# Kernel tuning notes

Hardware: AMD Instinct MI355X
Metric: run time of the kernel (lower is better)

Reference implementation:

```python
import jax, jax.numpy as jnp
import numpy as np

N_NODES, N_FEAT, N_HID, N_CLS = 50000, 128, 64, 16
N_EDGES, N_EDGES2 = 800000, 3000000


def _rand_edges(key, n_edges, n_nodes):
    # self-loop-free random edge list [2, E] (src, dst)
    k1, k2 = jax.random.split(key)
    src = jax.random.randint(k1, (n_edges,), 0, n_nodes)
    off = jax.random.randint(k2, (n_edges,), 1, n_nodes)
    dst = (src + off) % n_nodes
    return jnp.stack([src, dst]).astype(jnp.int64)


def setup_inputs() -> dict:
    key = jax.random.key(0)
    ks = jax.random.split(key, 8)
    x = jax.random.normal(ks[0], (N_NODES, N_FEAT), jnp.float32)
    edge_index = _rand_edges(ks[1], N_EDGES, N_NODES)    # original edges, no self loops
    edge_index2 = _rand_edges(ks[2], N_EDGES2, N_NODES)  # exclusive 2-hop edges
    w1 = jax.random.normal(ks[3], (N_FEAT, N_HID), jnp.float32) / np.sqrt(N_FEAT)
    b1 = jnp.zeros((N_HID,), jnp.float32)
    w2 = jax.random.normal(ks[4], (3 * N_HID, N_CLS), jnp.float32) / np.sqrt(3 * N_HID)
    b2 = jnp.zeros((N_CLS,), jnp.float32)
    lin_w = jax.random.normal(ks[5], (3 * N_CLS, N_CLS), jnp.float32) / np.sqrt(3 * N_CLS)
    lin_b = jnp.zeros((N_CLS,), jnp.float32)
    return {"x": x, "w1": w1, "b1": b1, "w2": w2, "b2": b2,
            "lin_w": lin_w, "lin_b": lin_b,
            "edge_index": edge_index, "edge_index2": edge_index2}


def _gcn_conv(h, W, b, ei, n):
    # PyG GCNConv(add_self_loops=False): transform, symmetric-normalize, scatter-add, bias.
    hw = h @ W                                   # [n, d_out]
    src, dst = ei[0], ei[1]
    ones = jnp.ones(ei.shape[1], h.dtype)
    deg = jax.ops.segment_sum(ones, dst, num_segments=n)       # in-degree
    dinv = jnp.where(deg > 0, jax.lax.rsqrt(jnp.maximum(deg, 1e-12)), 0.0)
    norm = dinv[src] * dinv[dst]                 # [E]
    msg = hw[src] * norm[:, None]                # gather + scale (traffic-bound)
    return jax.ops.segment_sum(msg, dst, num_segments=n) + b


def reference(x, w1, b1, w2, b2, lin_w, lin_b, edge_index, edge_index2):
    n = x.shape[0]
    # layer 1: three branches over (original edges, 2-hop edges, self-loop-only)
    h1 = _gcn_conv(x, w1, b1, edge_index, n)
    h1_2 = _gcn_conv(x, w1, b1, edge_index2, n)
    h1_3 = x @ w1 + b1                           # self-loop-only GCN: deg=1, norm=1
    R1 = jax.nn.relu(jnp.concatenate([h1, h1_2, h1_3], axis=1))  # dropout = identity (eval)
    # layer 2: same three branches with shared gcn2 weights
    h2 = _gcn_conv(R1, w2, b2, edge_index, n)
    h2_2 = _gcn_conv(R1, w2, b2, edge_index2, n)
    h2_3 = R1 @ w2 + b2
    R2 = jnp.concatenate([h2, h2_2, h2_3], axis=1)
    out = R2 @ lin_w + lin_b
    return jax.nn.log_softmax(out, axis=1)
```

## Files before the change

### kernel.cpp

```cpp
#include <hip/hip_runtime.h>
#include <math.h>


#define NPB    64
#define CHUNK  8192
#define HCHUNK 16384

typedef unsigned short us8 __attribute__((ext_vector_type(8)));

__device__ inline float b2f(unsigned short u) {
    return __uint_as_float(((unsigned int)u) << 16);
}
__device__ inline unsigned short f2b(float f) {
    unsigned int u = __float_as_uint(f);
    u = (u + 0x7FFFu + ((u >> 16) & 1u)) >> 16;
    return (unsigned short)u;
}

__global__ void __launch_bounds__(256)
k_gemm1(const float* __restrict__ x, const float* __restrict__ w1,
        unsigned short* __restrict__ hwb, int n) {
    __shared__ float ws[128 * 64];
    __shared__ float xs[64 * 128];
    int t = threadIdx.x;
    int row0 = blockIdx.x * 64;
    for (int i = t; i < 128 * 16; i += 256)
        ((float4*)ws)[i] = ((const float4*)w1)[i];
    for (int i = t; i < 64 * 32; i += 256) {
        int r = row0 + (i >> 5);
        ((float4*)xs)[i] = (r < n) ? ((const float4*)x)[r * 32 + (i & 31)]
                                   : make_float4(0.f, 0.f, 0.f, 0.f);
    }
    __syncthreads();
    int tr = t >> 4, tc = t & 15;
    float acc[4][4] = {};
    #pragma unroll 4
    for (int k4 = 0; k4 < 32; ++k4) {
        float4 wv0 = *(const float4*)&ws[(k4 * 4 + 0) * 64 + tc * 4];
        float4 wv1 = *(const float4*)&ws[(k4 * 4 + 1) * 64 + tc * 4];
        float4 wv2 = *(const float4*)&ws[(k4 * 4 + 2) * 64 + tc * 4];
        float4 wv3 = *(const float4*)&ws[(k4 * 4 + 3) * 64 + tc * 4];
        #pragma unroll
        for (int r = 0; r < 4; ++r) {
            float4 xv = *(const float4*)&xs[(tr * 4 + r) * 128 + k4 * 4];
            acc[r][0] = fmaf(xv.x, wv0.x, acc[r][0]);
            acc[r][1] = fmaf(xv.x, wv0.y, acc[r][1]);
            acc[r][2] = fmaf(xv.x, wv0.z, acc[r][2]);
            acc[r][3] = fmaf(xv.x, wv0.w, acc[r][3]);
            acc[r][0] = fmaf(xv.y, wv1.x, acc[r][0]);
            acc[r][1] = fmaf(xv.y, wv1.y, acc[r][1]);
            acc[r][2] = fmaf(xv.y, wv1.z, acc[r][2]);
            acc[r][3] = fmaf(xv.y, wv1.w, acc[r][3]);
            acc[r][0] = fmaf(xv.z, wv2.x, acc[r][0]);
            acc[r][1] = fmaf(xv.z, wv2.y, acc[r][1]);
            acc[r][2] = fmaf(xv.z, wv2.z, acc[r][2]);
            acc[r][3] = fmaf(xv.z, wv2.w, acc[r][3]);
            acc[r][0] = fmaf(xv.w, wv3.x, acc[r][0]);
            acc[r][1] = fmaf(xv.w, wv3.y, acc[r][1]);
            acc[r][2] = fmaf(xv.w, wv3.z, acc[r][2]);
            acc[r][3] = fmaf(xv.w, wv3.w, acc[r][3]);
        }
    }
    #pragma unroll
    for (int r = 0; r < 4; ++r) {
        int rr = row0 + tr * 4 + r;
        if (rr < n) {
            ushort4 o;
            o.x = f2b(acc[r][0]); o.y = f2b(acc[r][1]);
            o.z = f2b(acc[r][2]); o.w = f2b(acc[r][3]);
            *(ushort4*)&hwb[rr * 64 + tc * 4] = o;
        }
    }
}

__global__ void k_hist2(const int* __restrict__ dstA, int* __restrict__ bhA, int EA, int nbA,
                        const int* __restrict__ dstB, int* __restrict__ bhB, int EB) {
    __shared__ int lh[1024];
    const int* dst; int* bh; int E; int cb;
    if ((int)blockIdx.x < nbA) { dst = dstA; bh = bhA; E = EA; cb = blockIdx.x; }
    else                       { dst = dstB; bh = bhB; E = EB; cb = blockIdx.x - nbA; }
    int t = threadIdx.x;
    for (int i = t; i < 1024; i += 256) lh[i] = 0;
    __syncthreads();
    int base = cb * HCHUNK;
    int cnt = min(HCHUNK, E - base);
    for (int i = t; i < cnt; i += 256) atomicAdd(&lh[dst[base + i] >> 6], 1);
    __syncthreads();
    for (int b = t; b < 1024; b += 256)
        if (lh[b]) atomicAdd(&bh[b], lh[b]);
}

__global__ void k_bscan(const int* __restrict__ bhA, int* __restrict__ bbA, int* __restrict__ bcA,
                        const int* __restrict__ bhB, int* __restrict__ bbB, int* __restrict__ bcB,
                        int B) {
    const int* bh = blockIdx.x ? bhB : bhA;
    int* bb = blockIdx.x ? bbB : bbA;
    int* bc = blockIdx.x ? bcB : bcA;
    int t = threadIdx.x;
    int carry = 0;
    int nch = (B + 63) >> 6;
    for (int c = 0; c < nch; ++c) {
        int idx = c * 64 + t;
        int v = (idx < B) ? bh[idx] : 0;
        int incl = v;
        #pragma unroll
        for (int off = 1; off < 64; off <<= 1) {
            int tv = __shfl_up(incl, off);
            if (t >= off) incl += tv;
        }
        if (idx < B) { bb[idx] = incl - v + carry; bc[idx] = incl - v + carry; }
        carry += __shfl(incl, 63);
    }
    if (t == 0) bb[B] = carry;
}

__global__ void __launch_bounds__(256)
k_part2(const int* __restrict__ srcA, const int* __restrict__ dstA,
        int* __restrict__ bcurA, unsigned int* __restrict__ outA, int EA, int nbA,
        const int* __restrict__ srcB, const int* __restrict__ dstB,
        int* __restrict__ bcurB, unsigned int* __restrict__ outB, int EB) {
    __shared__ int lh[1024];
    __shared__ int loff[1024];
    __shared__ int gof[1024];
    __shared__ int lcur[1024];
    __shared__ unsigned int stage[CHUNK];
    const int *src, *dst; int *bcur; unsigned int *out; int E, cb;
    if ((int)blockIdx.x < nbA) { src = srcA; dst = dstA; bcur = bcurA; out = outA; E = EA; cb = blockIdx.x; }
    else                       { src = srcB; dst = dstB; bcur = bcurB; out = outB; E = EB; cb = blockIdx.x - nbA; }
    int t = threadIdx.x;
    int base = cb * CHUNK;
    int cnt = min(CHUNK, E - base);
    for (int i = t; i < 1024; i += 256) lh[i] = 0;
    __syncthreads();
    for (int i = t; i < cnt; i += 256) atomicAdd(&lh[dst[base + i] >> 6], 1);
    __syncthreads();
    if (t < 64) {
        int carry = 0;
        #pragma unroll
        for (int c = 0; c < 16; ++c) {
            int idx = c * 64 + t;
            int v = lh[idx];
            int incl = v;
            #pragma unroll
            for (int off = 1; off < 64; off <<= 1) {
                int tv = __shfl_up(incl, off);
                if (t >= off) incl += tv;
            }
            loff[idx] = incl - v + carry;
            carry += __shfl(incl, 63);
        }
    }
    __syncthreads();
    for (int b = t; b < 1024; b += 256) {
        int c = lh[b];
        gof[b] = c ? atomicAdd(&bcur[b], c) : 0;
        lcur[b] = loff[b];
    }
    __syncthreads();
    for (int i = t; i < cnt; i += 256) {
        int d = dst[base + i];
        int s = src[base + i];
        int bkt = d >> 6;
        int p = atomicAdd(&lcur[bkt], 1);
        stage[p] = (unsigned int)s | ((unsigned int)(d & 63) << 16) |
                   ((unsigned int)bkt << 22);
    }
    __syncthreads();
    for (int i = t; i < cnt; i += 256) {
        unsigned int e = stage[i];
        int bkt = (int)(e >> 22);
        out[gof[bkt] + (i - loff[bkt])] = e & 0x3FFFFFu;
    }
}

__global__ void __launch_bounds__(256)
k_csr2(const int* __restrict__ bbaseA, const unsigned int* __restrict__ ebufA,
       int* __restrict__ rsA, float* __restrict__ dvA, unsigned short* __restrict__ ssrcA, int EA,
       const int* __restrict__ bbaseB, const unsigned int* __restrict__ ebufB,
       int* __restrict__ rsB, float* __restrict__ dvB, unsigned short* __restrict__ ssrcB, int EB,
       int B, int n) {
    __shared__ int cnt[64];
    __shared__ int lcur[64];
    const int* bbase; const unsigned int* ebuf; int* rs; float* dv;
    unsigned short* ssrc; int b, Etot;
    if ((int)blockIdx.x < B) { bbase = bbaseA; ebuf = ebufA; rs = rsA; dv = dvA; ssrc = ssrcA; b = blockIdx.x; Etot = EA; }
    else                     { bbase = bbaseB; ebuf = ebufB; rs = rsB; dv = dvB; ssrc = ssrcB; b = blockIdx.x - B; Etot = EB; }
    int t = threadIdx.x;
    if (t < 64) cnt[t] = 0;
    __syncthreads();
    int beg = bbase[b], end = bbase[b + 1];
    for (int i = beg + t; i < end; i += 256)
        atomicAdd(&cnt[(ebuf[i] >> 16) & 63u], 1);
    __syncthreads();
    if (t < 64) {
        int v = cnt[t];
        int incl = v;
        #pragma unroll
        for (int off = 1; off < 64; off <<= 1) {
            int tv = __shfl_up(incl, off);
            if (t >= off) incl += tv;
        }
        int start = beg + incl - v;
        lcur[t] = start;
        int node = b * NPB + t;
        if (node < n) {
            rs[node] = start;
            dv[node] = (v > 0) ? rsqrtf((float)v) : 0.f;
        }
    }
    __syncthreads();
    for (int i = beg + t; i < end; i += 256) {
        unsigned int e = ebuf[i];
        int p = atomicAdd(&lcur[(e >> 16) & 63u], 1);
        ssrc[p] = (unsigned short)(e & 0xFFFFu);
    }
    if (t == 0 && b == B - 1) rs[n] = Etot;
}

__device__ inline void agg64_body(const int* __restrict__ rs,
                                  const unsigned short* __restrict__ ssrc,
                                  const float* __restrict__ dinv,
                                  const us8* __restrict__ hwb8,
                                  const float* __restrict__ b1,
                                  unsigned short* __restrict__ R1b,
                                  int col_unit, int n, int tid) {
    int v = tid >> 3, q = tid & 7;
    if (v >= n) return;
    int beg = rs[v], end = rs[v + 1];
    float a[8] = {0.f, 0.f, 0.f, 0.f, 0.f, 0.f, 0.f, 0.f};
    int i = beg;
    for (; i + 8 <= end; i += 8) {
        int s0 = ssrc[i + 0], s1 = ssrc[i + 1], s2 = ssrc[i + 2], s3 = ssrc[i + 3];
        int s4 = ssrc[i + 4], s5 = ssrc[i + 5], s6 = ssrc[i + 6], s7 = ssrc[i + 7];
        float c0 = dinv[s0], c1 = dinv[s1], c2 = dinv[s2], c3 = dinv[s3];
        float c4 = dinv[s4], c5 = dinv[s5], c6 = dinv[s6], c7 = dinv[s7];
        us8 h0 = hwb8[s0 * 8 + q], h1 = hwb8[s1 * 8 + q];
        us8 h2 = hwb8[s2 * 8 + q], h3 = hwb8[s3 * 8 + q];
        us8 h4 = hwb8[s4 * 8 + q], h5 = hwb8[s5 * 8 + q];
        us8 h6 = hwb8[s6 * 8 + q], h7 = hwb8[s7 * 8 + q];
        #pragma unroll
        for (int j = 0; j < 8; ++j) {
            a[j] = fmaf(b2f(h0[j]), c0, a[j]);
            a[j] = fmaf(b2f(h1[j]), c1, a[j]);
            a[j] = fmaf(b2f(h2[j]), c2, a[j]);
            a[j] = fmaf(b2f(h3[j]), c3, a[j]);
            a[j] = fmaf(b2f(h4[j]), c4, a[j]);
            a[j] = fmaf(b2f(h5[j]), c5, a[j]);
            a[j] = fmaf(b2f(h6[j]), c6, a[j]);
            a[j] = fmaf(b2f(h7[j]), c7, a[j]);
        }
    }
    for (; i < end; ++i) {
        int s = ssrc[i];
        float sc = dinv[s];
        us8 h = hwb8[s * 8 + q];
        #pragma unroll
        for (int j = 0; j < 8; ++j) a[j] = fmaf(b2f(h[j]), sc, a[j]);
    }
    float dd = dinv[v];
    us8 o;
    #pragma unroll
    for (int j = 0; j < 8; ++j) {
        float r = fmaf(a[j], dd, b1[q * 8 + j]);
        o[j] = f2b(r > 0.f ? r : 0.f);
    }
    ((us8*)&R1b[v * 192])[col_unit + q] = o;
}

__global__ void k_agg1f(const int* __restrict__ rs1, const unsigned short* __restrict__ ssrc1,
                        const float* __restrict__ dinv1,
                        const int* __restrict__ rs2, const unsigned short* __restrict__ ssrc2,
                        const float* __restrict__ dinv2,
                        const us8* __restrict__ hwb8, const float* __restrict__ b1,
                        unsigned short* __restrict__ R1b, int n, int nba) {
    int bid = blockIdx.x;
    if (bid < nba) {
        agg64_body(rs2, ssrc2, dinv2, hwb8, b1, R1b, 8, n, bid * 256 + threadIdx.x);
    } else if (bid < 2 * nba) {
        agg64_body(rs1, ssrc1, dinv1, hwb8, b1, R1b, 0, n,
                   (bid - nba) * 256 + threadIdx.x);
    } else {
        int tid = (bid - 2 * nba) * 256 + threadIdx.x;
        int v = tid >> 3, q = tid & 7;
        if (v >= n) return;
        us8 h = hwb8[v * 8 + q];
        us8 o;
        #pragma unroll
        for (int j = 0; j < 8; ++j) {
            float r = b2f(h[j]) + b1[q * 8 + j];
            o[j] = f2b(r > 0.f ? r : 0.f);
        }
        ((us8*)&R1b[v * 192])[16 + q] = o;
    }
}

__global__ void __launch_bounds__(256)
k_gemm2(const unsigned short* __restrict__ R1b, const float* __restrict__ w2,
        unsigned short* __restrict__ hwb2, int n) {
    __shared__ float ws[192 * 16];
    __shared__ float rs[16][193];
    int t = threadIdx.x;
    for (int i = t; i < 192 * 16; i += 256) ws[i] = w2[i];
    int row0 = blockIdx.x * 16;
    for (int i = t; i < 16 * 192; i += 256) {
        int r = i / 192, j = i - r * 192;
        int v = row0 + r;
        rs[r][j] = (v < n) ? b2f(R1b[v * 192 + j]) : 0.f;
    }
    __syncthreads();
    int r = t >> 4, c = t & 15;
    int v = row0 + r;
    if (v >= n) return;
    float acc = 0.f;
    #pragma unroll 8
    for (int j = 0; j < 192; ++j) acc += rs[r][j] * ws[j * 16 + c];
    hwb2[v * 16 + c] = f2b(acc);
}

__device__ inline void agg16_body(const int* __restrict__ rs,
                                  const unsigned short* __restrict__ ssrc,
                                  const float* __restrict__ dinv,
                                  const us8* __restrict__ hwb2_8,
                                  float* __restrict__ acc2, int n, int tid) {
    int v = tid >> 1, q = tid & 1;
    if (v >= n) return;
    int beg = rs[v], end = rs[v + 1];
    float a[8] = {0.f, 0.f, 0.f, 0.f, 0.f, 0.f, 0.f, 0.f};
    int i = beg;
    for (; i + 8 <= end; i += 8) {
        int s0 = ssrc[i + 0], s1 = ssrc[i + 1], s2 = ssrc[i + 2], s3 = ssrc[i + 3];
        int s4 = ssrc[i + 4], s5 = ssrc[i + 5], s6 = ssrc[i + 6], s7 = ssrc[i + 7];
        float c0 = dinv[s0], c1 = dinv[s1], c2 = dinv[s2], c3 = dinv[s3];
        float c4 = dinv[s4], c5 = dinv[s5], c6 = dinv[s6], c7 = dinv[s7];
        us8 h0 = hwb2_8[s0 * 2 + q], h1 = hwb2_8[s1 * 2 + q];
        us8 h2 = hwb2_8[s2 * 2 + q], h3 = hwb2_8[s3 * 2 + q];
        us8 h4 = hwb2_8[s4 * 2 + q], h5 = hwb2_8[s5 * 2 + q];
        us8 h6 = hwb2_8[s6 * 2 + q], h7 = hwb2_8[s7 * 2 + q];
        #pragma unroll
        for (int j = 0; j < 8; ++j) {
            a[j] = fmaf(b2f(h0[j]), c0, a[j]);
            a[j] = fmaf(b2f(h1[j]), c1, a[j]);
            a[j] = fmaf(b2f(h2[j]), c2, a[j]);
            a[j] = fmaf(b2f(h3[j]), c3, a[j]);
            a[j] = fmaf(b2f(h4[j]), c4, a[j]);
            a[j] = fmaf(b2f(h5[j]), c5, a[j]);
            a[j] = fmaf(b2f(h6[j]), c6, a[j]);
            a[j] = fmaf(b2f(h7[j]), c7, a[j]);
        }
    }
    for (; i < end; ++i) {
        int s = ssrc[i];
        float sc = dinv[s];
        us8 h = hwb2_8[s * 2 + q];
        #pragma unroll
        for (int j = 0; j < 8; ++j) a[j] = fmaf(b2f(h[j]), sc, a[j]);
    }
    float4* o = (float4*)&acc2[v * 16 + q * 8];
    o[0] = make_float4(a[0], a[1], a[2], a[3]);
    o[1] = make_float4(a[4], a[5], a[6], a[7]);
}

__global__ void k_agg16f(const int* __restrict__ rs1, const unsigned short* __restrict__ ssrc1,
                         const float* __restrict__ dinv1, float* __restrict__ acc2a,
                         const int* __restrict__ rs2, const unsigned short* __restrict__ ssrc2,
                         const float* __restrict__ dinv2, float* __restrict__ acc2b,
                         const us8* __restrict__ hwb2_8, int n, int nba) {
    int bid = blockIdx.x;
    if (bid < nba)
        agg16_body(rs2, ssrc2, dinv2, hwb2_8, acc2b, n, bid * 256 + threadIdx.x);
    else
        agg16_body(rs1, ssrc1, dinv1, hwb2_8, acc2a, n, (bid - nba) * 256 + threadIdx.x);
}

__global__ void k_final(const unsigned short* __restrict__ hwb2,
                        const float* __restrict__ acc2a, const float* __restrict__ acc2b,
                        const float* __restrict__ dinv1, const float* __restrict__ dinv2,
                        const float* __restrict__ b2, const float* __restrict__ lw,
                        const float* __restrict__ lb, float* __restrict__ out, int n) {
    __shared__ float lws[48 * 16];
    __shared__ float r2s[16][49];
    int t = threadIdx.x;
    for (int i = t; i < 48 * 16; i += 256) lws[i] = lw[i];
    int ni = t >> 4, c = t & 15;
    int v = blockIdx.x * 16 + ni;
    if (v < n) {
        float bb = b2[c];
        r2s[ni][c]      = fmaf(dinv1[v], acc2a[v * 16 + c], bb);
        r2s[ni][16 + c] = fmaf(dinv2[v], acc2b[v * 16 + c], bb);
        r2s[ni][32 + c] = b2f(hwb2[v * 16 + c]) + bb;
    }
    __syncthreads();
    if (v >= n) return;
    float o = lb[c];
    #pragma unroll
    for (int j = 0; j < 48; ++j) o += r2s[ni][j] * lws[j * 16 + c];
    float m = o;
    for (int off = 8; off >= 1; off >>= 1) m = fmaxf(m, __shfl_xor(m, off, 16));
    float e = expf(o - m);
    float ssum = e;
    for (int off = 8; off >= 1; off >>= 1) ssum += __shfl_xor(ssum, off, 16);
    out[v * 16 + c] = (o - m) - logf(ssum);
}

extern "C" void kernel_launch(void* const* d_in, const int* in_sizes, int n_in,
                              void* d_out, int out_size, void* d_ws, size_t ws_size,
                              hipStream_t stream) {
    const float* x     = (const float*)d_in[0];
    const float* w1    = (const float*)d_in[1];
    const float* b1    = (const float*)d_in[2];
    const float* w2    = (const float*)d_in[3];
    const float* b2    = (const float*)d_in[4];
    const float* lin_w = (const float*)d_in[5];
    const float* lin_b = (const float*)d_in[6];
    const int*   ei    = (const int*)d_in[7];
    const int*   ei2   = (const int*)d_in[8];

    const int n  = in_sizes[0] / 128;
    const int E1 = in_sizes[7] / 2;
    const int E2 = in_sizes[8] / 2;
    const int B  = (n + NPB - 1) / NPB;

    char* ws = (char*)d_ws;
    unsigned short* hwb   = (unsigned short*)(ws + 0);
    unsigned short* hwb2  = (unsigned short*)(ws + 6400000);
    unsigned short* R1b   = (unsigned short*)(ws + 8000000);
    unsigned short* ssrc1 = (unsigned short*)(ws + 27200000);
    unsigned short* ssrc2 = (unsigned short*)(ws + 28800000);
    unsigned int* ebuf1   = (unsigned int*)(ws + 34800000);
    unsigned int* ebuf2   = (unsigned int*)(ws + 38000000);
    float*        acc2a   = (float*)(ws + 50000000);
    float*        acc2b   = (float*)(ws + 53200000);
    float*        dinv1   = (float*)(ws + 56800000);
    float*        dinv2   = (float*)(ws + 57000000);
    int*          rs1     = (int*)(ws + 57200000);
    int*          rs2     = (int*)(ws + 57400016);
    int*          bhist1  = (int*)(ws + 58000032);
    int*          bhist2  = (int*)(ws + 58004128);
    int*          bbase1  = (int*)(ws + 58008224);
    int*          bbase2  = (int*)(ws + 58012320);
    int*          bcur1   = (int*)(ws + 58016416);
    int*          bcur2   = (int*)(ws + 58020512);

    hipMemsetAsync(bhist1, 0, 8192, stream);

    k_gemm1<<<(n + 63) / 64, 256, 0, stream>>>(x, w1, hwb, n);

    const int nbh1 = (E1 + HCHUNK - 1) / HCHUNK, nbh2 = (E2 + HCHUNK - 1) / HCHUNK;
    k_hist2<<<nbh1 + nbh2, 256, 0, stream>>>(ei + E1, bhist1, E1, nbh1,
                                             ei2 + E2, bhist2, E2);
    k_bscan<<<2, 64, 0, stream>>>(bhist1, bbase1, bcur1, bhist2, bbase2, bcur2, B);

    const int nbp1 = (E1 + CHUNK - 1) / CHUNK, nbp2 = (E2 + CHUNK - 1) / CHUNK;
    k_part2<<<nbp1 + nbp2, 256, 0, stream>>>(ei, ei + E1, bcur1, ebuf1, E1, nbp1,
                                             ei2, ei2 + E2, bcur2, ebuf2, E2);

    k_csr2<<<2 * B, 256, 0, stream>>>(bbase1, ebuf1, rs1, dinv1, ssrc1, E1,
                                      bbase2, ebuf2, rs2, dinv2, ssrc2, E2, B, n);

    const int nba = (n * 8 + 255) / 256;
    k_agg1f<<<3 * nba, 256, 0, stream>>>(rs1, ssrc1, dinv1, rs2, ssrc2, dinv2,
                                         (const us8*)hwb, b1, R1b, n, nba);

    k_gemm2<<<(n + 15) / 16, 256, 0, stream>>>(R1b, w2, hwb2, n);

    const int nb16 = (n * 2 + 255) / 256;
    k_agg16f<<<2 * nb16, 256, 0, stream>>>(rs1, ssrc1, dinv1, acc2a,
                                           rs2, ssrc2, dinv2, acc2b,
                                           (const us8*)hwb2, n, nb16);

    k_final<<<(n + 15) / 16, 256, 0, stream>>>(hwb2, acc2a, acc2b, dinv1, dinv2, b2,
                                               lin_w, lin_b, (float*)d_out, n);
}
```

Before: 259.8 us.

## Fuse layer-2 aggregation with final linear, widen partition blocks, vectorize index loads

Merges the layer-2 16-wide aggregation and the final linear/log-softmax into one kernel that holds per-node accumulators in shared memory, removing the acc2 global round trip and one launch. The partition kernel now uses 1024 threads with chunks twice as large, and its bucket scan is parallelised across warps. The gather loops peel up to an 8-aligned boundary so source indices can be read with one 16-byte vector load. The fused kernel uses fewer blocks than the separate aggregation kernel, which may reduce latency hiding on the gather.

```diff
diff --git a/kernel.cpp b/kernel.cpp
--- a/kernel.cpp
+++ b/kernel.cpp
@@ -3,7 +3,7 @@
 
 
 #define NPB    64
-#define CHUNK  8192
+#define CHUNK  16384
 #define HCHUNK 16384
 
 typedef unsigned short us8 __attribute__((ext_vector_type(8)));
@@ -114,7 +114,7 @@
     if (t == 0) bb[B] = carry;
 }
 
-__global__ void __launch_bounds__(256)
+__global__ void __launch_bounds__(1024)
 k_part2(const int* __restrict__ srcA, const int* __restrict__ dstA,
         int* __restrict__ bcurA, unsigned int* __restrict__ outA, int EA, int nbA,
         const int* __restrict__ srcB, const int* __restrict__ dstB,
@@ -130,34 +130,37 @@
     int t = threadIdx.x;
     int base = cb * CHUNK;
     int cnt = min(CHUNK, E - base);
-    for (int i = t; i < 1024; i += 256) lh[i] = 0;
-    __syncthreads();
-    for (int i = t; i < cnt; i += 256) atomicAdd(&lh[dst[base + i] >> 6], 1);
-    __syncthreads();
-    if (t < 64) {
-        int carry = 0;
-        #pragma unroll
-        for (int c = 0; c < 16; ++c) {
-            int idx = c * 64 + t;
-            int v = lh[idx];
-            int incl = v;
-            #pragma unroll
-            for (int off = 1; off < 64; off <<= 1) {
-                int tv = __shfl_up(incl, off);
-                if (t >= off) incl += tv;
-            }
-            loff[idx] = incl - v + carry;
-            carry += __shfl(incl, 63);
-        }
-    }
-    __syncthreads();
-    for (int b = t; b < 1024; b += 256) {
-        int c = lh[b];
-        gof[b] = c ? atomicAdd(&bcur[b], c) : 0;
-        lcur[b] = loff[b];
-    }
-    __syncthreads();
-    for (int i = t; i < cnt; i += 256) {
+    lh[t] = 0;
+    __syncthreads();
+    for (int i = t; i < cnt; i += 1024) atomicAdd(&lh[dst[base + i] >> 6], 1);
+    __syncthreads();
+    int vdeg = lh[t];
+    int incl = vdeg;
+    #pragma unroll
+    for (int off = 1; off < 64; off <<= 1) {
+        int tv = __shfl_up(incl, off);
+        if ((t & 63) >= off) incl += tv;
+    }
+    if ((t & 63) == 63) gof[t >> 6] = incl;
+    __syncthreads();
+    if (t < 16) {
+        int wv = gof[t];
+        int winc = wv;
+        #pragma unroll
+        for (int off = 1; off < 16; off <<= 1) {
+            int tv = __shfl_up(winc, off, 16);
+            if (t >= off) winc += tv;
+        }
+        gof[16 + t] = winc - wv;
+    }
+    __syncthreads();
+    int excl = incl - vdeg + gof[16 + (t >> 6)];
+    loff[t] = excl;
+    lcur[t] = excl;
+    __syncthreads();
+    gof[t] = vdeg ? atomicAdd(&bcur[t], vdeg) : 0;
+    __syncthreads();
+    for (int i = t; i < cnt; i += 1024) {
         int d = dst[base + i];
         int s = src[base + i];
         int bkt = d >> 6;
@@ -166,7 +169,7 @@
                    ((unsigned int)bkt << 22);
     }
     __syncthreads();
-    for (int i = t; i < cnt; i += 256) {
+    for (int i = t; i < cnt; i += 1024) {
         unsigned int e = stage[i];
         int bkt = (int)(e >> 22);
         out[gof[bkt] + (i - loff[bkt])] = e & 0x3FFFFFu;
@@ -229,9 +232,19 @@
     int beg = rs[v], end = rs[v + 1];
     float a[8] = {0.f, 0.f, 0.f, 0.f, 0.f, 0.f, 0.f, 0.f};
     int i = beg;
+    int al = (beg + 7) & ~7;
+    int stop = (al < end) ? al : end;
+    for (; i < stop; ++i) {
+        int s = ssrc[i];
+        float sc = dinv[s];
+        us8 h = hwb8[s * 8 + q];
+        #pragma unroll
+        for (int j = 0; j < 8; ++j) a[j] = fmaf(b2f(h[j]), sc, a[j]);
+    }
     for (; i + 8 <= end; i += 8) {
-        int s0 = ssrc[i + 0], s1 = ssrc[i + 1], s2 = ssrc[i + 2], s3 = ssrc[i + 3];
-        int s4 = ssrc[i + 4], s5 = ssrc[i + 5], s6 = ssrc[i + 6], s7 = ssrc[i + 7];
+        us8 sv = *(const us8*)(ssrc + i);
+        int s0 = sv[0], s1 = sv[1], s2 = sv[2], s3 = sv[3];
+        int s4 = sv[4], s5 = sv[5], s6 = sv[6], s7 = sv[7];
         float c0 = dinv[s0], c1 = dinv[s1], c2 = dinv[s2], c3 = dinv[s3];
         float c4 = dinv[s4], c5 = dinv[s5], c6 = dinv[s6], c7 = dinv[s7];
         us8 h0 = hwb8[s0 * 8 + q], h1 = hwb8[s1 * 8 + q];
@@ -317,25 +330,34 @@
     hwb2[v * 16 + c] = f2b(acc);
 }
 
-__device__ inline void agg16_body(const int* __restrict__ rs,
-                                  const unsigned short* __restrict__ ssrc,
-                                  const float* __restrict__ dinv,
-                                  const us8* __restrict__ hwb2_8,
-                                  float* __restrict__ acc2, int n, int tid) {
-    int v = tid >> 1, q = tid & 1;
-    if (v >= n) return;
+__device__ inline void gath16(const int* __restrict__ rs,
+                              const unsigned short* __restrict__ ssrc,
+                              const float* __restrict__ dinv,
+                              const us8* __restrict__ h8,
+                              int v, int q, float* __restrict__ a) {
     int beg = rs[v], end = rs[v + 1];
-    float a[8] = {0.f, 0.f, 0.f, 0.f, 0.f, 0.f, 0.f, 0.f};
+    #pragma unroll
+    for (int j = 0; j < 8; ++j) a[j] = 0.f;
     int i = beg;
+    int al = (beg + 7) & ~7;
+    int stop = (al < end) ? al : end;
+    for (; i < stop; ++i) {
+        int s = ssrc[i];
+        float sc = dinv[s];
+        us8 h = h8[s * 2 + q];
+        #pragma unroll
+        for (int j = 0; j < 8; ++j) a[j] = fmaf(b2f(h[j]), sc, a[j]);
+    }
     for (; i + 8 <= end; i += 8) {
-        int s0 = ssrc[i + 0], s1 = ssrc[i + 1], s2 = ssrc[i + 2], s3 = ssrc[i + 3];
-        int s4 = ssrc[i + 4], s5 = ssrc[i + 5], s6 = ssrc[i + 6], s7 = ssrc[i + 7];
+        us8 sv = *(const us8*)(ssrc + i);
+        int s0 = sv[0], s1 = sv[1], s2 = sv[2], s3 = sv[3];
+        int s4 = sv[4], s5 = sv[5], s6 = sv[6], s7 = sv[7];
         float c0 = dinv[s0], c1 = dinv[s1], c2 = dinv[s2], c3 = dinv[s3];
         float c4 = dinv[s4], c5 = dinv[s5], c6 = dinv[s6], c7 = dinv[s7];
-        us8 h0 = hwb2_8[s0 * 2 + q], h1 = hwb2_8[s1 * 2 + q];
-        us8 h2 = hwb2_8[s2 * 2 + q], h3 = hwb2_8[s3 * 2 + q];
-        us8 h4 = hwb2_8[s4 * 2 + q], h5 = hwb2_8[s5 * 2 + q];
-        us8 h6 = hwb2_8[s6 * 2 + q], h7 = hwb2_8[s7 * 2 + q];
+        us8 h0 = h8[s0 * 2 + q], h1 = h8[s1 * 2 + q];
+        us8 h2 = h8[s2 * 2 + q], h3 = h8[s3 * 2 + q];
+        us8 h4 = h8[s4 * 2 + q], h5 = h8[s5 * 2 + q];
+        us8 h6 = h8[s6 * 2 + q], h7 = h8[s7 * 2 + q];
         #pragma unroll
         for (int j = 0; j < 8; ++j) {
             a[j] = fmaf(b2f(h0[j]), c0, a[j]);
@@ -351,55 +373,63 @@
     for (; i < end; ++i) {
         int s = ssrc[i];
         float sc = dinv[s];
-        us8 h = hwb2_8[s * 2 + q];
+        us8 h = h8[s * 2 + q];
         #pragma unroll
         for (int j = 0; j < 8; ++j) a[j] = fmaf(b2f(h[j]), sc, a[j]);
     }
-    float4* o = (float4*)&acc2[v * 16 + q * 8];
-    o[0] = make_float4(a[0], a[1], a[2], a[3]);
-    o[1] = make_float4(a[4], a[5], a[6], a[7]);
-}
-
-__global__ void k_agg16f(const int* __restrict__ rs1, const unsigned short* __restrict__ ssrc1,
-                         const float* __restrict__ dinv1, float* __restrict__ acc2a,
-                         const int* __restrict__ rs2, const unsigned short* __restrict__ ssrc2,
-                         const float* __restrict__ dinv2, float* __restrict__ acc2b,
-                         const us8* __restrict__ hwb2_8, int n, int nba) {
-    int bid = blockIdx.x;
-    if (bid < nba)
-        agg16_body(rs2, ssrc2, dinv2, hwb2_8, acc2b, n, bid * 256 + threadIdx.x);
-    else
-        agg16_body(rs1, ssrc1, dinv1, hwb2_8, acc2a, n, (bid - nba) * 256 + threadIdx.x);
-}
-
-__global__ void k_final(const unsigned short* __restrict__ hwb2,
-                        const float* __restrict__ acc2a, const float* __restrict__ acc2b,
-                        const float* __restrict__ dinv1, const float* __restrict__ dinv2,
-                        const float* __restrict__ b2, const float* __restrict__ lw,
-                        const float* __restrict__ lb, float* __restrict__ out, int n) {
+}
+
+__global__ void __launch_bounds__(256)
+k_l2f(const int* __restrict__ rs1, const unsigned short* __restrict__ ssrc1,
+      const float* __restrict__ dinv1,
+      const int* __restrict__ rs2, const unsigned short* __restrict__ ssrc2,
+      const float* __restrict__ dinv2,
+      const us8* __restrict__ hwb2_8, const unsigned short* __restrict__ hwb2,
+      const float* __restrict__ b2, const float* __restrict__ lw,
+      const float* __restrict__ lb, float* __restrict__ out, int n) {
+    __shared__ float accA[128 * 16];
+    __shared__ float accB[128 * 16];
     __shared__ float lws[48 * 16];
     __shared__ float r2s[16][49];
     int t = threadIdx.x;
+    int v0 = blockIdx.x * 128;
     for (int i = t; i < 48 * 16; i += 256) lws[i] = lw[i];
+    int vl = t >> 1, q = t & 1;
+    int v = v0 + vl;
+    if (v < n) {
+        float a[8];
+        gath16(rs2, ssrc2, dinv2, hwb2_8, v, q, a);
+        #pragma unroll
+        for (int j = 0; j < 8; ++j) accB[vl * 16 + q * 8 + j] = a[j];
+        gath16(rs1, ssrc1, dinv1, hwb2_8, v, q, a);
+        #pragma unroll
+        for (int j = 0; j < 8; ++j) accA[vl * 16 + q * 8 + j] = a[j];
+    }
+    __syncthreads();
     int ni = t >> 4, c = t & 15;
-    int v = blockIdx.x * 16 + ni;
-    if (v < n) {
-        float bb = b2[c];
-        r2s[ni][c]      = fmaf(dinv1[v], acc2a[v * 16 + c], bb);
-        r2s[ni][16 + c] = fmaf(dinv2[v], acc2b[v * 16 + c], bb);
-        r2s[ni][32 + c] = b2f(hwb2[v * 16 + c]) + bb;
-    }
-    __syncthreads();
-    if (v >= n) return;
-    float o = lb[c];
-    #pragma unroll
-    for (int j = 0; j < 48; ++j) o += r2s[ni][j] * lws[j * 16 + c];
-    float m = o;
-    for (int off = 8; off >= 1; off >>= 1) m = fmaxf(m, __shfl_xor(m, off, 16));
-    float e = expf(o - m);
-    float ssum = e;
-    for (int off = 8; off >= 1; off >>= 1) ssum += __shfl_xor(ssum, off, 16);
-    out[v * 16 + c] = (o - m) - logf(ssum);
+    for (int p = 0; p < 8; ++p) {
+        int vv = v0 + p * 16 + ni;
+        int vl2 = p * 16 + ni;
+        if (vv < n) {
+            float bb = b2[c];
+            r2s[ni][c]      = fmaf(dinv1[vv], accA[vl2 * 16 + c], bb);
+            r2s[ni][16 + c] = fmaf(dinv2[vv], accB[vl2 * 16 + c], bb);
+            r2s[ni][32 + c] = b2f(hwb2[vv * 16 + c]) + bb;
+        }
+        __syncthreads();
+        if (vv < n) {
+            float o = lb[c];
+            #pragma unroll
+            for (int j = 0; j < 48; ++j) o += r2s[ni][j] * lws[j * 16 + c];
+            float m = o;
+            for (int off = 8; off >= 1; off >>= 1) m = fmaxf(m, __shfl_xor(m, off, 16));
+            float e = expf(o - m);
+            float ssum = e;
+            for (int off = 8; off >= 1; off >>= 1) ssum += __shfl_xor(ssum, off, 16);
+            out[vv * 16 + c] = (o - m) - logf(ssum);
+        }
+        __syncthreads();
+    }
 }
 
 extern "C" void kernel_launch(void* const* d_in, const int* in_sizes, int n_in,
@@ -428,8 +458,6 @@
     unsigned short* ssrc2 = (unsigned short*)(ws + 28800000);
     unsigned int* ebuf1   = (unsigned int*)(ws + 34800000);
     unsigned int* ebuf2   = (unsigned int*)(ws + 38000000);
-    float*        acc2a   = (float*)(ws + 50000000);
-    float*        acc2b   = (float*)(ws + 53200000);
     float*        dinv1   = (float*)(ws + 56800000);
     float*        dinv2   = (float*)(ws + 57000000);
     int*          rs1     = (int*)(ws + 57200000);
@@ -451,8 +479,8 @@
     k_bscan<<<2, 64, 0, stream>>>(bhist1, bbase1, bcur1, bhist2, bbase2, bcur2, B);
 
     const int nbp1 = (E1 + CHUNK - 1) / CHUNK, nbp2 = (E2 + CHUNK - 1) / CHUNK;
-    k_part2<<<nbp1 + nbp2, 256, 0, stream>>>(ei, ei + E1, bcur1, ebuf1, E1, nbp1,
-                                             ei2, ei2 + E2, bcur2, ebuf2, E2);
+    k_part2<<<nbp1 + nbp2, 1024, 0, stream>>>(ei, ei + E1, bcur1, ebuf1, E1, nbp1,
+                                              ei2, ei2 + E2, bcur2, ebuf2, E2);
 
     k_csr2<<<2 * B, 256, 0, stream>>>(bbase1, ebuf1, rs1, dinv1, ssrc1, E1,
                                       bbase2, ebuf2, rs2, dinv2, ssrc2, E2, B, n);
@@ -463,11 +491,7 @@
 
     k_gemm2<<<(n + 15) / 16, 256, 0, stream>>>(R1b, w2, hwb2, n);
 
-    const int nb16 = (n * 2 + 255) / 256;
-    k_agg16f<<<2 * nb16, 256, 0, stream>>>(rs1, ssrc1, dinv1, acc2a,
-                                           rs2, ssrc2, dinv2, acc2b,
-                                           (const us8*)hwb2, n, nb16);
-
-    k_final<<<(n + 15) / 16, 256, 0, stream>>>(hwb2, acc2a, acc2b, dinv1, dinv2, b2,
+    k_l2f<<<(n + 127) / 128, 256, 0, stream>>>(rs1, ssrc1, dinv1, rs2, ssrc2, dinv2,
+                                               (const us8*)hwb2, hwb2, b2,
                                                lin_w, lin_b, (float*)d_out, n);
 }
```

After: 253.4 us. 1.03x faster.
